# Kernel optimization log

Measured on AMD Instinct MI355X. Metric: run time of the kernel, lower is better.

## Reference

```python
import jax, jax.numpy as jnp
import numpy as np

NEG_SLOPE = 0.01  # torch nn.LeakyReLU default


def setup_inputs() -> dict:
    key = jax.random.key(0)
    k1, k2, k3 = jax.random.split(key, 3)
    B, H, D, L = 4, 8, 64, 2048
    q = jax.random.normal(k1, (B, H, D, L), dtype=jnp.float32)
    k = jax.random.normal(k2, (B, H, D, L), dtype=jnp.float32)
    v = jax.random.normal(k3, (B, H, D, L), dtype=jnp.float32)
    return {"q": q, "k": k, "v": v}


def reference(q, k, v):
    # q, k, v: [B, H, D, L] (note: feature dim BEFORE length, as in the torch module)
    d_tensor = q.shape[2]
    scale = 1.0 / np.sqrt(d_tensor).astype(np.float32)
    # scores = LeakyReLU(q^T k / sqrt(d)) : [B, H, Lq, Lk]
    scores = jnp.einsum('bhdq,bhdk->bhqk', q, k) * scale
    scores = jax.nn.leaky_relu(scores, negative_slope=NEG_SLOPE)
    psi = jax.nn.softmax(scores, axis=-1)
    # out = (psi @ v^T)^T : [B, H, D, Lq]
    out = jnp.einsum('bhqk,bhdk->bhdq', psi, v)
    return out
```

## Files before the change

kernel.cpp:

```cpp
#include <hip/hip_runtime.h>
#include <math.h>

#define DD 64
#define LL 2048
#define HEADS 32
#define TQ 128
#define TK 64
#define NTHREADS 512
#define QSCALE 0.18033688011112042f

typedef __bf16 bf16_t;
typedef __bf16 bf16x8 __attribute__((ext_vector_type(8)));
typedef float f32x16 __attribute__((ext_vector_type(16)));

__global__ __launch_bounds__(256)
void prep_bf16_kv(const float* __restrict__ k, const float* __restrict__ v,
                  bf16_t* __restrict__ kt, bf16_t* __restrict__ vb) {
  __shared__ float ld[64][65];
  const int t = threadIdx.x;
  const int which = blockIdx.z;
  const int head = blockIdx.y;
  const int l0 = blockIdx.x * 64;
  const size_t hoff = (size_t)head * DD * LL;
  if (which == 1) {
    const float* src = v + hoff;
    bf16_t* dst = vb + hoff;
    const int lp = (t & 31) * 2;
    const int db = (t >> 5) * 8;
    for (int i = 0; i < 8; ++i) {
      int d = db + i;
      float2 x = *(const float2*)(src + (size_t)d * LL + l0 + lp);
      union { bf16_t b[2]; unsigned u; } pk;
      pk.b[0] = (bf16_t)x.x;
      pk.b[1] = (bf16_t)x.y;
      *(unsigned*)(dst + (size_t)d * LL + l0 + lp) = pk.u;
    }
  } else {
    const float* src = k + hoff;
    bf16_t* dst = kt + hoff;
    const int l = t & 63;
    const int db = (t >> 6) * 16;
    for (int i = 0; i < 16; ++i) {
      int d = db + i;
      ld[l][d] = src[(size_t)d * LL + l0 + l];
    }
    __syncthreads();
    const int dp = (t & 31) * 2;
    const int lb = (t >> 5) * 8;
    for (int i = 0; i < 8; ++i) {
      int lw = lb + i;
      union { bf16_t b[2]; unsigned u; } pk;
      pk.b[0] = (bf16_t)ld[lw][dp];
      pk.b[1] = (bf16_t)ld[lw][dp + 1];
      *(unsigned*)(dst + (size_t)(l0 + lw) * DD + dp) = pk.u;
    }
  }
}

struct __align__(16) SMemA4 {
  union {
    bf16_t Qs[TQ][72];
    bf16_t Ks[2][TK][72];
  } qk;
  bf16_t Vs[2][DD][72];
};
union __align__(16) SMemU4 {
  SMemA4 a;
  float Oe[TQ][65];
};

__global__ __launch_bounds__(NTHREADS, 4)
void attn_flash_bf16_v5(const float* __restrict__ q, const bf16_t* __restrict__ kt,
                        const bf16_t* __restrict__ vb, float* __restrict__ out) {
  __shared__ SMemU4 sm;
  __shared__ float rs1[TQ];
  const int tid  = threadIdx.x;
  const int w    = tid >> 6;
  const int lane = tid & 63;
  const int l31  = lane & 31;
  const int hh   = lane >> 5;
  const int strip = w & 3;
  const int half  = w >> 2;
  const int wbase = strip * 32;
  const int lkh   = half * 32;
  const int bid  = blockIdx.x;
  const int j    = bid >> 3;
  const int head = (bid & 7) + 8 * (j >> 4);
  const int q0   = (j & 15) * TQ;
  const size_t hoff = (size_t)head * DD * LL;
  const float*  qp = q  + hoff;
  const bf16_t* kp = kt + hoff;
  const bf16_t* vp = vb + hoff;

  const int srow = tid >> 3;
  const int scol = (tid & 7) * 8;

  bf16x8 kreg = *(const bf16x8*)(kp + (size_t)srow * DD + scol);
  bf16x8 vreg = *(const bf16x8*)(vp + (size_t)srow * LL + scol);

  {
    int lq  = tid & 127;
    int d0q = (tid >> 7) * 16;
    const float* src = qp + q0 + lq;
    for (int g = 0; g < 2; ++g) {
      bf16x8 pk;
      for (int jj = 0; jj < 8; ++jj)
        pk[jj] = (bf16_t)(src[(size_t)(d0q + g * 8 + jj) * LL] * QSCALE);
      *(bf16x8*)&sm.a.qk.Qs[lq][d0q + g * 8] = pk;
    }
  }

  __syncthreads();
  bf16x8 bq[4];
  for (int kk = 0; kk < 4; ++kk)
    bq[kk] = *(const bf16x8*)&sm.a.qk.Qs[wbase + l31][kk * 16 + 8 * hh];
  __syncthreads();

  f32x16 oacc[2];
  for (int dt = 0; dt < 2; ++dt)
    for (int r = 0; r < 16; ++r) oacc[dt][r] = 0.f;
  float rsl[4];
  for (int i = 0; i < 4; ++i) rsl[i] = 0.f;

  for (int t = 0; t < LL / TK; ++t) {
    const int cur = t & 1;
    *(bf16x8*)&sm.a.qk.Ks[cur][srow][scol] = kreg;
    *(bf16x8*)&sm.a.Vs[cur][srow][scol]    = vreg;
    __syncthreads();

    if (t + 1 < LL / TK) {
      const int lk0n = (t + 1) * TK;
      kreg = *(const bf16x8*)(kp + (size_t)(lk0n + srow) * DD + scol);
      vreg = *(const bf16x8*)(vp + (size_t)srow * LL + lk0n + scol);
    }

    f32x16 st;
    for (int r = 0; r < 16; ++r) st[r] = 0.f;
    __builtin_amdgcn_s_setprio(1);
    for (int kk = 0; kk < 4; ++kk) {
      bf16x8 ak = *(const bf16x8*)&sm.a.qk.Ks[cur][lkh + l31][kk * 16 + 8 * hh];
      st = __builtin_amdgcn_mfma_f32_32x32x16_bf16(ak, bq[kk], st, 0, 0, 0);
    }
    __builtin_amdgcn_s_setprio(0);

    unsigned pb[8];
#pragma unroll
    for (int r = 0; r < 16; ++r) {
      float s = st[r];
      s = fmaxf(s, 0.01f * s);
      float p = __builtin_amdgcn_exp2f(s);
      rsl[r & 3] += p;
      st[r] = p;
    }
    for (int qq = 0; qq < 8; ++qq) {
      union { bf16_t b[2]; unsigned u; } pk;
      pk.b[0] = (bf16_t)st[2 * qq];
      pk.b[1] = (bf16_t)st[2 * qq + 1];
      pb[qq] = pk.u;
    }

    for (int kk2 = 0; kk2 < 2; ++kk2) {
      unsigned l0 = pb[4 * kk2 + 0], l1 = pb[4 * kk2 + 1];
      unsigned l2 = pb[4 * kk2 + 2], l3 = pb[4 * kk2 + 3];
      unsigned s0 = hh ? l0 : l2;
      unsigned s1 = hh ? l1 : l3;
      unsigned f0 = (unsigned)__shfl_xor((int)s0, 32);
      unsigned f1 = (unsigned)__shfl_xor((int)s1, 32);
      union { unsigned u[4]; bf16x8 v; } ap;
      ap.u[0] = hh ? f0 : l0;
      ap.u[1] = hh ? f1 : l1;
      ap.u[2] = hh ? l2 : f0;
      ap.u[3] = hh ? l3 : f1;
      const int lkb = lkh + kk2 * 16 + 8 * hh;
      __builtin_amdgcn_s_setprio(1);
      for (int dt = 0; dt < 2; ++dt) {
        bf16x8 bv = *(const bf16x8*)&sm.a.Vs[cur][dt * 32 + l31][lkb];
        oacc[dt] = __builtin_amdgcn_mfma_f32_32x32x16_bf16(ap.v, bv, oacc[dt], 0, 0, 0);
      }
      __builtin_amdgcn_s_setprio(0);
    }
  }

  float rsum = (rsl[0] + rsl[1]) + (rsl[2] + rsl[3]);
  float rtot = rsum + __shfl_xor(rsum, 32);
  __syncthreads();
  if (half == 1) {
    rs1[wbase + l31] = rtot;
    for (int r = 0; r < 16; ++r) {
      int row = (r & 3) + 8 * (r >> 2) + 4 * hh;
      for (int dt = 0; dt < 2; ++dt)
        sm.Oe[wbase + row][dt * 32 + l31] = oacc[dt][r];
    }
  }
  __syncthreads();
  if (half == 0) {
    float tot = rtot + rs1[wbase + l31];
    rs1[wbase + l31] = 1.0f / tot;
    float inv[16];
    for (int r = 0; r < 16; ++r) {
      int row = (r & 3) + 8 * (r >> 2) + 4 * hh;
      inv[r] = rs1[wbase + row];
    }
    for (int r = 0; r < 16; ++r) {
      int row = (r & 3) + 8 * (r >> 2) + 4 * hh;
      for (int dt = 0; dt < 2; ++dt) {
        int col = dt * 32 + l31;
        sm.Oe[wbase + row][col] = (oacc[dt][r] + sm.Oe[wbase + row][col]) * inv[r];
      }
    }
  }
  __syncthreads();
  float* op = out + hoff + q0;
  for (int i = 0; i < 16; ++i) {
    int idx = tid + NTHREADS * i;
    int d   = idx >> 7;
    int lq  = idx & 127;
    op[(size_t)d * LL + lq] = sm.Oe[lq][d];
  }
}

struct __align__(16) SMemA {
  bf16_t Qs[TQ][72];
  bf16_t Ks[TK][72];
  bf16_t Vs[DD][72];
};
union __align__(16) SMemU {
  SMemA a;
  float Oe[TQ][65];
};

__global__ __launch_bounds__(NTHREADS, 4)
void attn_flash_bf16(const float* __restrict__ q, const float* __restrict__ k,
                     const float* __restrict__ v, float* __restrict__ out) {
  __shared__ SMemU sm;
  __shared__ float rs1[TQ];
  const int tid  = threadIdx.x;
  const int w    = tid >> 6;
  const int lane = tid & 63;
  const int l31  = lane & 31;
  const int hh   = lane >> 5;
  const int strip = w & 3;
  const int half  = w >> 2;
  const int wbase = strip * 32;
  const int lkh   = half * 32;
  const int head = blockIdx.y;
  const int q0   = blockIdx.x * TQ;
  const size_t hoff = (size_t)head * DD * LL;
  const float* qp = q + hoff;
  const float* kp = k + hoff;
  const float* vp = v + hoff;

  {
    int lq  = tid & 127;
    int d0q = (tid >> 7) * 16;
    const float* src = qp + q0 + lq;
    for (int g = 0; g < 2; ++g) {
      bf16x8 pk;
      for (int jj = 0; jj < 8; ++jj)
        pk[jj] = (bf16_t)(src[(size_t)(d0q + g * 8 + jj) * LL] * QSCALE);
      *(bf16x8*)&sm.a.Qs[lq][d0q + g * 8] = pk;
    }
  }

  const int klk = tid & 63;
  const int kd0 = (tid >> 6) * 8;
  const int vd  = tid >> 3;
  const int vc8 = (tid & 7) * 8;

  float  kreg[8];
  float4 vreg[2];
  {
    const float* ks = kp + klk;
    for (int jj = 0; jj < 8; ++jj) kreg[jj] = ks[(size_t)(kd0 + jj) * LL];
    vreg[0] = *(const float4*)(vp + (size_t)vd * LL + vc8);
    vreg[1] = *(const float4*)(vp + (size_t)vd * LL + vc8 + 4);
  }

  __syncthreads();
  bf16x8 bq[4];
  for (int kk = 0; kk < 4; ++kk)
    bq[kk] = *(const bf16x8*)&sm.a.Qs[wbase + l31][kk * 16 + 8 * hh];

  f32x16 oacc[2];
  for (int dt = 0; dt < 2; ++dt)
    for (int r = 0; r < 16; ++r) oacc[dt][r] = 0.f;
  float rsum = 0.f;

  for (int t = 0; t < LL / TK; ++t) {
    __syncthreads();
    {
      bf16x8 pk;
      for (int jj = 0; jj < 8; ++jj) pk[jj] = (bf16_t)kreg[jj];
      *(bf16x8*)&sm.a.Ks[klk][kd0] = pk;
      bf16x8 pv;
      pv[0] = (bf16_t)vreg[0].x; pv[1] = (bf16_t)vreg[0].y;
      pv[2] = (bf16_t)vreg[0].z; pv[3] = (bf16_t)vreg[0].w;
      pv[4] = (bf16_t)vreg[1].x; pv[5] = (bf16_t)vreg[1].y;
      pv[6] = (bf16_t)vreg[1].z; pv[7] = (bf16_t)vreg[1].w;
      *(bf16x8*)&sm.a.Vs[vd][vc8] = pv;
    }
    __syncthreads();

    if (t + 1 < LL / TK) {
      const int lk0n = (t + 1) * TK;
      const float* ks = kp + lk0n + klk;
      for (int jj = 0; jj < 8; ++jj) kreg[jj] = ks[(size_t)(kd0 + jj) * LL];
      vreg[0] = *(const float4*)(vp + (size_t)vd * LL + lk0n + vc8);
      vreg[1] = *(const float4*)(vp + (size_t)vd * LL + lk0n + vc8 + 4);
    }

    f32x16 st;
    for (int r = 0; r < 16; ++r) st[r] = 0.f;
    for (int kk = 0; kk < 4; ++kk) {
      bf16x8 ak = *(const bf16x8*)&sm.a.Ks[lkh + l31][kk * 16 + 8 * hh];
      st = __builtin_amdgcn_mfma_f32_32x32x16_bf16(ak, bq[kk], st, 0, 0, 0);
    }

    unsigned pb[8];
    for (int r = 0; r < 16; ++r) {
      float s = st[r];
      s = fmaxf(s, 0.01f * s);
      float p = __builtin_amdgcn_exp2f(s);
      rsum += p;
      st[r] = p;
    }
    for (int qq = 0; qq < 8; ++qq) {
      union { bf16_t b[2]; unsigned u; } pk;
      pk.b[0] = (bf16_t)st[2 * qq];
      pk.b[1] = (bf16_t)st[2 * qq + 1];
      pb[qq] = pk.u;
    }

    for (int kk2 = 0; kk2 < 2; ++kk2) {
      unsigned l0 = pb[4 * kk2 + 0], l1 = pb[4 * kk2 + 1];
      unsigned l2 = pb[4 * kk2 + 2], l3 = pb[4 * kk2 + 3];
      unsigned s0 = hh ? l0 : l2;
      unsigned s1 = hh ? l1 : l3;
      unsigned f0 = (unsigned)__shfl_xor((int)s0, 32);
      unsigned f1 = (unsigned)__shfl_xor((int)s1, 32);
      union { unsigned u[4]; bf16x8 v; } ap;
      ap.u[0] = hh ? f0 : l0;
      ap.u[1] = hh ? f1 : l1;
      ap.u[2] = hh ? l2 : f0;
      ap.u[3] = hh ? l3 : f1;
      const int lkb = lkh + kk2 * 16 + 8 * hh;
      for (int dt = 0; dt < 2; ++dt) {
        bf16x8 bv = *(const bf16x8*)&sm.a.Vs[dt * 32 + l31][lkb];
        oacc[dt] = __builtin_amdgcn_mfma_f32_32x32x16_bf16(ap.v, bv, oacc[dt], 0, 0, 0);
      }
    }
  }

  float rtot = rsum + __shfl_xor(rsum, 32);
  __syncthreads();
  if (half == 1) {
    rs1[wbase + l31] = rtot;
    for (int r = 0; r < 16; ++r) {
      int row = (r & 3) + 8 * (r >> 2) + 4 * hh;
      for (int dt = 0; dt < 2; ++dt)
        sm.Oe[wbase + row][dt * 32 + l31] = oacc[dt][r];
    }
  }
  __syncthreads();
  if (half == 0) {
    float tot = rtot + rs1[wbase + l31];
    rs1[wbase + l31] = 1.0f / tot;
    float inv[16];
    for (int r = 0; r < 16; ++r) {
      int row = (r & 3) + 8 * (r >> 2) + 4 * hh;
      inv[r] = rs1[wbase + row];
    }
    for (int r = 0; r < 16; ++r) {
      int row = (r & 3) + 8 * (r >> 2) + 4 * hh;
      for (int dt = 0; dt < 2; ++dt) {
        int col = dt * 32 + l31;
        sm.Oe[wbase + row][col] = (oacc[dt][r] + sm.Oe[wbase + row][col]) * inv[r];
      }
    }
  }
  __syncthreads();
  float* op = out + hoff + q0;
  for (int i = 0; i < 16; ++i) {
    int idx = tid + NTHREADS * i;
    int d   = idx >> 7;
    int lq  = idx & 127;
    op[(size_t)d * LL + lq] = sm.Oe[lq][d];
  }
}

extern "C" void kernel_launch(void* const* d_in, const int* in_sizes, int n_in,
                              void* d_out, int out_size, void* d_ws, size_t ws_size,
                              hipStream_t stream) {
  const float* q = (const float*)d_in[0];
  const float* k = (const float*)d_in[1];
  const float* v = (const float*)d_in[2];
  float* out = (float*)d_out;
  const size_t per_buf = (size_t)HEADS * DD * LL;
  const size_t need = 2 * per_buf * sizeof(bf16_t);
  if (d_ws && ws_size >= need) {
    bf16_t* kt = (bf16_t*)d_ws;
    bf16_t* vb = kt + per_buf;
    prep_bf16_kv<<<dim3(LL / 64, HEADS, 2), 256, 0, stream>>>(k, v, kt, vb);
    attn_flash_bf16_v5<<<dim3((LL / TQ) * HEADS), NTHREADS, 0, stream>>>(q, kt, vb, out);
  } else {
    attn_flash_bf16<<<dim3(LL / TQ, HEADS), NTHREADS, 0, stream>>>(q, k, v, out);
  }
}
```

Before: 143.9 us.

## Split key dimension across two blocks and combine partial outputs in separate kernel

Adds a split-K variant of the flash attention kernel. Each query tile's key range is divided into two halves handled by separate blocks, which write unnormalized partial outputs and row sums to workspace. A new combine kernel adds the two partials, normalizes, and writes the transposed output. This doubles the block count (512 -> 1024) to improve occupancy across the CUs, at the cost of extra workspace traffic and an additional kernel launch. It relies on the no-max softmax (LeakyReLU scores are bounded), so the partials can be summed without rescaling.

```diff
diff --git a/kernel.cpp b/kernel.cpp
--- a/kernel.cpp
+++ b/kernel.cpp
@@ -7,6 +7,8 @@
 #define TQ 128
 #define TK 64
 #define NTHREADS 512
+#define NQT (LL / TQ)
+#define KHALF (LL / 2)
 #define QSCALE 0.18033688011112042f
 
 typedef __bf16 bf16_t;
@@ -68,6 +70,188 @@
   SMemA4 a;
   float Oe[TQ][65];
 };
+
+__global__ __launch_bounds__(NTHREADS, 4)
+void attn_flash_splitk(const float* __restrict__ q, const bf16_t* __restrict__ kt,
+                       const bf16_t* __restrict__ vb, float* __restrict__ po,
+                       float* __restrict__ pr) {
+  __shared__ SMemU4 sm;
+  __shared__ float rs1[TQ];
+  const int tid  = threadIdx.x;
+  const int w    = tid >> 6;
+  const int lane = tid & 63;
+  const int l31  = lane & 31;
+  const int hh   = lane >> 5;
+  const int strip = w & 3;
+  const int half  = w >> 2;
+  const int wbase = strip * 32;
+  const int lkh   = half * 32;
+  const int bid  = blockIdx.x;
+  const int j    = bid >> 3;
+  const int kp   = j & 1;
+  const int qt   = (j >> 1) & 15;
+  const int head = (bid & 7) + 8 * (j >> 5);
+  const int q0   = qt * TQ;
+  const int kbase = kp * KHALF;
+  const size_t hoff = (size_t)head * DD * LL;
+  const float*  qp = q  + hoff;
+  const bf16_t* kpt = kt + hoff;
+  const bf16_t* vp = vb + hoff;
+  const int b2 = ((head << 4) + qt) * 2 + kp;
+
+  const int srow = tid >> 3;
+  const int scol = (tid & 7) * 8;
+
+  bf16x8 kreg = *(const bf16x8*)(kpt + (size_t)(kbase + srow) * DD + scol);
+  bf16x8 vreg = *(const bf16x8*)(vp + (size_t)srow * LL + kbase + scol);
+
+  {
+    int lq  = tid & 127;
+    int d0q = (tid >> 7) * 16;
+    const float* src = qp + q0 + lq;
+    for (int g = 0; g < 2; ++g) {
+      bf16x8 pk;
+      for (int jj = 0; jj < 8; ++jj)
+        pk[jj] = (bf16_t)(src[(size_t)(d0q + g * 8 + jj) * LL] * QSCALE);
+      *(bf16x8*)&sm.a.qk.Qs[lq][d0q + g * 8] = pk;
+    }
+  }
+
+  __syncthreads();
+  bf16x8 bq[4];
+  for (int kk = 0; kk < 4; ++kk)
+    bq[kk] = *(const bf16x8*)&sm.a.qk.Qs[wbase + l31][kk * 16 + 8 * hh];
+  __syncthreads();
+
+  f32x16 oacc[2];
+  for (int dt = 0; dt < 2; ++dt)
+    for (int r = 0; r < 16; ++r) oacc[dt][r] = 0.f;
+  float rsl[4];
+  for (int i = 0; i < 4; ++i) rsl[i] = 0.f;
+
+  for (int t = 0; t < KHALF / TK; ++t) {
+    const int cur = t & 1;
+    *(bf16x8*)&sm.a.qk.Ks[cur][srow][scol] = kreg;
+    *(bf16x8*)&sm.a.Vs[cur][srow][scol]    = vreg;
+    __syncthreads();
+
+    if (t + 1 < KHALF / TK) {
+      const int lk0n = kbase + (t + 1) * TK;
+      kreg = *(const bf16x8*)(kpt + (size_t)(lk0n + srow) * DD + scol);
+      vreg = *(const bf16x8*)(vp + (size_t)srow * LL + lk0n + scol);
+    }
+
+    f32x16 st;
+    for (int r = 0; r < 16; ++r) st[r] = 0.f;
+    __builtin_amdgcn_s_setprio(1);
+    for (int kk = 0; kk < 4; ++kk) {
+      bf16x8 ak = *(const bf16x8*)&sm.a.qk.Ks[cur][lkh + l31][kk * 16 + 8 * hh];
+      st = __builtin_amdgcn_mfma_f32_32x32x16_bf16(ak, bq[kk], st, 0, 0, 0);
+    }
+    __builtin_amdgcn_s_setprio(0);
+
+    unsigned pb[8];
+#pragma unroll
+    for (int r = 0; r < 16; ++r) {
+      float s = st[r];
+      s = fmaxf(s, 0.01f * s);
+      float p = __builtin_amdgcn_exp2f(s);
+      rsl[r & 3] += p;
+      st[r] = p;
+    }
+    for (int qq = 0; qq < 8; ++qq) {
+      union { bf16_t b[2]; unsigned u; } pk;
+      pk.b[0] = (bf16_t)st[2 * qq];
+      pk.b[1] = (bf16_t)st[2 * qq + 1];
+      pb[qq] = pk.u;
+    }
+
+    for (int kk2 = 0; kk2 < 2; ++kk2) {
+      unsigned l0 = pb[4 * kk2 + 0], l1 = pb[4 * kk2 + 1];
+      unsigned l2 = pb[4 * kk2 + 2], l3 = pb[4 * kk2 + 3];
+      unsigned s0 = hh ? l0 : l2;
+      unsigned s1 = hh ? l1 : l3;
+      unsigned f0 = (unsigned)__shfl_xor((int)s0, 32);
+      unsigned f1 = (unsigned)__shfl_xor((int)s1, 32);
+      union { unsigned u[4]; bf16x8 v; } ap;
+      ap.u[0] = hh ? f0 : l0;
+      ap.u[1] = hh ? f1 : l1;
+      ap.u[2] = hh ? l2 : f0;
+      ap.u[3] = hh ? l3 : f1;
+      const int lkb = lkh + kk2 * 16 + 8 * hh;
+      __builtin_amdgcn_s_setprio(1);
+      for (int dt = 0; dt < 2; ++dt) {
+        bf16x8 bv = *(const bf16x8*)&sm.a.Vs[cur][dt * 32 + l31][lkb];
+        oacc[dt] = __builtin_amdgcn_mfma_f32_32x32x16_bf16(ap.v, bv, oacc[dt], 0, 0, 0);
+      }
+      __builtin_amdgcn_s_setprio(0);
+    }
+  }
+
+  float rsum = (rsl[0] + rsl[1]) + (rsl[2] + rsl[3]);
+  float rtot = rsum + __shfl_xor(rsum, 32);
+  __syncthreads();
+  if (half == 1) {
+    rs1[wbase + l31] = rtot;
+    for (int r = 0; r < 16; ++r) {
+      int row = (r & 3) + 8 * (r >> 2) + 4 * hh;
+      for (int dt = 0; dt < 2; ++dt)
+        sm.Oe[wbase + row][dt * 32 + l31] = oacc[dt][r];
+    }
+  }
+  __syncthreads();
+  if (half == 0) {
+    float tot = rtot + rs1[wbase + l31];
+    if (hh == 0) pr[(size_t)b2 * TQ + wbase + l31] = tot;
+    for (int r = 0; r < 16; ++r) {
+      int row = (r & 3) + 8 * (r >> 2) + 4 * hh;
+      for (int dt = 0; dt < 2; ++dt) {
+        int col = dt * 32 + l31;
+        sm.Oe[wbase + row][col] = oacc[dt][r] + sm.Oe[wbase + row][col];
+      }
+    }
+  }
+  __syncthreads();
+  float* pop = po + (size_t)b2 * (TQ * DD);
+  for (int i = 0; i < 16; ++i) {
+    int idx = tid + NTHREADS * i;
+    int lq = idx >> 6;
+    int d  = idx & 63;
+    pop[idx] = sm.Oe[lq][d];
+  }
+}
+
+__global__ __launch_bounds__(256)
+void combine_splitk(const float* __restrict__ po, const float* __restrict__ pr,
+                    float* __restrict__ out) {
+  __shared__ float Oe[TQ][65];
+  __shared__ float inv[TQ];
+  const int t = threadIdx.x;
+  const int b = blockIdx.x;
+  const int head = b >> 4;
+  const int q0   = (b & 15) * TQ;
+  const float* p0 = po + ((size_t)b * 2 + 0) * (TQ * DD);
+  const float* p1 = po + ((size_t)b * 2 + 1) * (TQ * DD);
+  for (int i = 0; i < (TQ * DD) / 256; ++i) {
+    int idx = t + 256 * i;
+    int lq = idx >> 6;
+    int d  = idx & 63;
+    Oe[lq][d] = p0[idx] + p1[idx];
+  }
+  if (t < TQ) {
+    const float* r0 = pr + ((size_t)b * 2 + 0) * TQ;
+    const float* r1 = pr + ((size_t)b * 2 + 1) * TQ;
+    inv[t] = 1.0f / (r0[t] + r1[t]);
+  }
+  __syncthreads();
+  float* op = out + (size_t)head * DD * LL + q0;
+  for (int i = 0; i < (TQ * DD) / 256; ++i) {
+    int idx = t + 256 * i;
+    int d  = idx >> 7;
+    int lq = idx & 127;
+    op[(size_t)d * LL + lq] = Oe[lq][d] * inv[lq];
+  }
+}
 
 __global__ __launch_bounds__(NTHREADS, 4)
 void attn_flash_bf16_v5(const float* __restrict__ q, const bf16_t* __restrict__ kt,
@@ -396,8 +580,19 @@
   const float* v = (const float*)d_in[2];
   float* out = (float*)d_out;
   const size_t per_buf = (size_t)HEADS * DD * LL;
-  const size_t need = 2 * per_buf * sizeof(bf16_t);
-  if (d_ws && ws_size >= need) {
+  const size_t kv_bytes = 2 * per_buf * sizeof(bf16_t);
+  const size_t po_elems = (size_t)HEADS * NQT * 2 * TQ * DD;
+  const size_t pr_elems = (size_t)HEADS * NQT * 2 * TQ;
+  const size_t need_full = kv_bytes + (po_elems + pr_elems) * sizeof(float);
+  if (d_ws && ws_size >= need_full) {
+    bf16_t* kt = (bf16_t*)d_ws;
+    bf16_t* vb = kt + per_buf;
+    float* po = (float*)((char*)d_ws + kv_bytes);
+    float* pr = po + po_elems;
+    prep_bf16_kv<<<dim3(LL / 64, HEADS, 2), 256, 0, stream>>>(k, v, kt, vb);
+    attn_flash_splitk<<<dim3(HEADS * NQT * 2), NTHREADS, 0, stream>>>(q, kt, vb, po, pr);
+    combine_splitk<<<dim3(HEADS * NQT), 256, 0, stream>>>(po, pr, out);
+  } else if (d_ws && ws_size >= kv_bytes) {
     bf16_t* kt = (bf16_t*)d_ws;
     bf16_t* vb = kt + per_buf;
     prep_bf16_kv<<<dim3(LL / 64, HEADS, 2), 256, 0, stream>>>(k, v, kt, vb);
```

Result: slower. 154.6 us (+7.4%).

## Load K/V MFMA fragments directly from global memory, dropping LDS staging

Applied to the files above, without the earlier changes.

The prep kernel now writes V in tiled 64x64 blocks, so each wave can fetch its MFMA operand fragments for K and V directly from global memory into registers. The attention loop no longer stages K/V tiles through shared memory and drops the per-iteration __syncthreads, prefetching the next tile's fragments into registers after the current MFMAs. Shared memory shrinks to the Q/output buffer, which may allow more resident blocks. The cost is that each of the 8 waves loads its own K/V fragments, adding redundant global/L2 traffic and more register pressure.

```diff
diff --git a/kernel.cpp b/kernel.cpp
--- a/kernel.cpp
+++ b/kernel.cpp
@@ -6,6 +6,7 @@
 #define HEADS 32
 #define TQ 128
 #define TK 64
+#define NT (LL / TK)
 #define NTHREADS 512
 #define QSCALE 0.18033688011112042f
 
@@ -14,8 +15,8 @@
 typedef float f32x16 __attribute__((ext_vector_type(16)));
 
 __global__ __launch_bounds__(256)
-void prep_bf16_kv(const float* __restrict__ k, const float* __restrict__ v,
-                  bf16_t* __restrict__ kt, bf16_t* __restrict__ vb) {
+void prep_bf16_kv2(const float* __restrict__ k, const float* __restrict__ v,
+                   bf16_t* __restrict__ kt, bf16_t* __restrict__ vt) {
   __shared__ float ld[64][65];
   const int t = threadIdx.x;
   const int which = blockIdx.z;
@@ -24,7 +25,7 @@
   const size_t hoff = (size_t)head * DD * LL;
   if (which == 1) {
     const float* src = v + hoff;
-    bf16_t* dst = vb + hoff;
+    bf16_t* dst = vt + hoff + (size_t)(l0 >> 6) * (DD * 64);
     const int lp = (t & 31) * 2;
     const int db = (t >> 5) * 8;
     for (int i = 0; i < 8; ++i) {
@@ -33,7 +34,7 @@
       union { bf16_t b[2]; unsigned u; } pk;
       pk.b[0] = (bf16_t)x.x;
       pk.b[1] = (bf16_t)x.y;
-      *(unsigned*)(dst + (size_t)d * LL + l0 + lp) = pk.u;
+      *(unsigned*)(dst + d * 64 + lp) = pk.u;
     }
   } else {
     const float* src = k + hoff;
@@ -57,22 +58,15 @@
   }
 }
 
-struct __align__(16) SMemA4 {
-  union {
-    bf16_t Qs[TQ][72];
-    bf16_t Ks[2][TK][72];
-  } qk;
-  bf16_t Vs[2][DD][72];
-};
-union __align__(16) SMemU4 {
-  SMemA4 a;
+union __align__(16) SMemU8 {
+  bf16_t Qs[TQ][72];
   float Oe[TQ][65];
 };
 
 __global__ __launch_bounds__(NTHREADS, 4)
-void attn_flash_bf16_v5(const float* __restrict__ q, const bf16_t* __restrict__ kt,
-                        const bf16_t* __restrict__ vb, float* __restrict__ out) {
-  __shared__ SMemU4 sm;
+void attn_flash_nolds(const float* __restrict__ q, const bf16_t* __restrict__ kt,
+                      const bf16_t* __restrict__ vt, float* __restrict__ out) {
+  __shared__ SMemU8 sm;
   __shared__ float rs1[TQ];
   const int tid  = threadIdx.x;
   const int w    = tid >> 6;
@@ -89,14 +83,17 @@
   const int q0   = (j & 15) * TQ;
   const size_t hoff = (size_t)head * DD * LL;
   const float*  qp = q  + hoff;
-  const bf16_t* kp = kt + hoff;
-  const bf16_t* vp = vb + hoff;
-
-  const int srow = tid >> 3;
-  const int scol = (tid & 7) * 8;
-
-  bf16x8 kreg = *(const bf16x8*)(kp + (size_t)srow * DD + scol);
-  bf16x8 vreg = *(const bf16x8*)(vp + (size_t)srow * LL + scol);
+
+  const bf16_t* kl = kt + hoff + (size_t)(lkh + l31) * 64 + hh * 8;
+  const bf16_t* vl = vt + hoff + (size_t)l31 * 64 + lkh + hh * 8;
+
+  bf16x8 ak[4], bv[4];
+#pragma unroll
+  for (int kk = 0; kk < 4; ++kk)
+    ak[kk] = *(const bf16x8*)(kl + kk * 16);
+#pragma unroll
+  for (int i = 0; i < 4; ++i)
+    bv[i] = *(const bf16x8*)(vl + (i >> 1) * 2048 + (i & 1) * 16);
 
   {
     int lq  = tid & 127;
@@ -106,15 +103,14 @@
       bf16x8 pk;
       for (int jj = 0; jj < 8; ++jj)
         pk[jj] = (bf16_t)(src[(size_t)(d0q + g * 8 + jj) * LL] * QSCALE);
-      *(bf16x8*)&sm.a.qk.Qs[lq][d0q + g * 8] = pk;
+      *(bf16x8*)&sm.Qs[lq][d0q + g * 8] = pk;
     }
   }
 
   __syncthreads();
   bf16x8 bq[4];
   for (int kk = 0; kk < 4; ++kk)
-    bq[kk] = *(const bf16x8*)&sm.a.qk.Qs[wbase + l31][kk * 16 + 8 * hh];
-  __syncthreads();
+    bq[kk] = *(const bf16x8*)&sm.Qs[wbase + l31][kk * 16 + 8 * hh];
 
   f32x16 oacc[2];
   for (int dt = 0; dt < 2; ++dt)
@@ -122,26 +118,19 @@
   float rsl[4];
   for (int i = 0; i < 4; ++i) rsl[i] = 0.f;
 
-  for (int t = 0; t < LL / TK; ++t) {
-    const int cur = t & 1;
-    *(bf16x8*)&sm.a.qk.Ks[cur][srow][scol] = kreg;
-    *(bf16x8*)&sm.a.Vs[cur][srow][scol]    = vreg;
-    __syncthreads();
-
-    if (t + 1 < LL / TK) {
-      const int lk0n = (t + 1) * TK;
-      kreg = *(const bf16x8*)(kp + (size_t)(lk0n + srow) * DD + scol);
-      vreg = *(const bf16x8*)(vp + (size_t)srow * LL + lk0n + scol);
-    }
+  for (int t = 0; t < NT; ++t) {
+    const int tn = (t + 1 < NT) ? t + 1 : t;
 
     f32x16 st;
     for (int r = 0; r < 16; ++r) st[r] = 0.f;
     __builtin_amdgcn_s_setprio(1);
-    for (int kk = 0; kk < 4; ++kk) {
-      bf16x8 ak = *(const bf16x8*)&sm.a.qk.Ks[cur][lkh + l31][kk * 16 + 8 * hh];
-      st = __builtin_amdgcn_mfma_f32_32x32x16_bf16(ak, bq[kk], st, 0, 0, 0);
-    }
+    for (int kk = 0; kk < 4; ++kk)
+      st = __builtin_amdgcn_mfma_f32_32x32x16_bf16(ak[kk], bq[kk], st, 0, 0, 0);
     __builtin_amdgcn_s_setprio(0);
+
+#pragma unroll
+    for (int kk = 0; kk < 4; ++kk)
+      ak[kk] = *(const bf16x8*)(kl + (size_t)tn * 4096 + kk * 16);
 
     unsigned pb[8];
 #pragma unroll
@@ -171,14 +160,16 @@
       ap.u[1] = hh ? f1 : l1;
       ap.u[2] = hh ? l2 : f0;
       ap.u[3] = hh ? l3 : f1;
-      const int lkb = lkh + kk2 * 16 + 8 * hh;
       __builtin_amdgcn_s_setprio(1);
-      for (int dt = 0; dt < 2; ++dt) {
-        bf16x8 bv = *(const bf16x8*)&sm.a.Vs[cur][dt * 32 + l31][lkb];
-        oacc[dt] = __builtin_amdgcn_mfma_f32_32x32x16_bf16(ap.v, bv, oacc[dt], 0, 0, 0);
-      }
+      for (int dt = 0; dt < 2; ++dt)
+        oacc[dt] = __builtin_amdgcn_mfma_f32_32x32x16_bf16(ap.v, bv[dt * 2 + kk2],
+                                                           oacc[dt], 0, 0, 0);
       __builtin_amdgcn_s_setprio(0);
     }
+
+#pragma unroll
+    for (int i = 0; i < 4; ++i)
+      bv[i] = *(const bf16x8*)(vl + (size_t)tn * 4096 + (i >> 1) * 2048 + (i & 1) * 16);
   }
 
   float rsum = (rsl[0] + rsl[1]) + (rsl[2] + rsl[3]);
@@ -312,8 +303,8 @@
     f32x16 st;
     for (int r = 0; r < 16; ++r) st[r] = 0.f;
     for (int kk = 0; kk < 4; ++kk) {
-      bf16x8 ak = *(const bf16x8*)&sm.a.Ks[lkh + l31][kk * 16 + 8 * hh];
-      st = __builtin_amdgcn_mfma_f32_32x32x16_bf16(ak, bq[kk], st, 0, 0, 0);
+      bf16x8 akf = *(const bf16x8*)&sm.a.Ks[lkh + l31][kk * 16 + 8 * hh];
+      st = __builtin_amdgcn_mfma_f32_32x32x16_bf16(akf, bq[kk], st, 0, 0, 0);
     }
 
     unsigned pb[8];
@@ -345,8 +336,8 @@
       ap.u[3] = hh ? l3 : f1;
       const int lkb = lkh + kk2 * 16 + 8 * hh;
       for (int dt = 0; dt < 2; ++dt) {
-        bf16x8 bv = *(const bf16x8*)&sm.a.Vs[dt * 32 + l31][lkb];
-        oacc[dt] = __builtin_amdgcn_mfma_f32_32x32x16_bf16(ap.v, bv, oacc[dt], 0, 0, 0);
+        bf16x8 bvf = *(const bf16x8*)&sm.a.Vs[dt * 32 + l31][lkb];
+        oacc[dt] = __builtin_amdgcn_mfma_f32_32x32x16_bf16(ap.v, bvf, oacc[dt], 0, 0, 0);
       }
     }
   }
@@ -399,9 +390,9 @@
   const size_t need = 2 * per_buf * sizeof(bf16_t);
   if (d_ws && ws_size >= need) {
     bf16_t* kt = (bf16_t*)d_ws;
-    bf16_t* vb = kt + per_buf;
-    prep_bf16_kv<<<dim3(LL / 64, HEADS, 2), 256, 0, stream>>>(k, v, kt, vb);
-    attn_flash_bf16_v5<<<dim3((LL / TQ) * HEADS), NTHREADS, 0, stream>>>(q, kt, vb, out);
+    bf16_t* vt = kt + per_buf;
+    prep_bf16_kv2<<<dim3(LL / 64, HEADS, 2), 256, 0, stream>>>(k, v, kt, vt);
+    attn_flash_nolds<<<dim3((LL / TQ) * HEADS), NTHREADS, 0, stream>>>(q, kt, vt, out);
   } else {
     attn_flash_bf16<<<dim3(LL / TQ, HEADS), NTHREADS, 0, stream>>>(q, k, v, out);
   }
```

Result: slower. 206.5 us (+43.5%).

## Software-pipeline QK^T one tile ahead of softmax and PV in flash kernel

Applied to the files above, without the earlier changes.

Restructures the main loop so that each iteration computes the QK^T scores for tile t while it applies softmax and the PV product to the scores of tile t-1. A prologue and an epilogue are added, and the V tile load lags K by one tile. The aim is to let the exp/pack VALU work and the PV MFMAs overlap with the next tile's score MFMAs and global loads. In exchange, a second 16-float score accumulator stays live, which raises register pressure and could hurt occupancy at 4 waves per SIMD.

```diff
diff --git a/kernel.cpp b/kernel.cpp
--- a/kernel.cpp
+++ b/kernel.cpp
@@ -6,6 +6,7 @@
 #define HEADS 32
 #define TQ 128
 #define TK 64
+#define NT (LL / TK)
 #define NTHREADS 512
 #define QSCALE 0.18033688011112042f
 
@@ -69,8 +70,51 @@
   float Oe[TQ][65];
 };
 
+#define SOFTMAX_PACK(STP, PB)                                  \
+  do {                                                         \
+    _Pragma("unroll")                                          \
+    for (int r = 0; r < 16; ++r) {                             \
+      float s = (STP)[r];                                      \
+      s = fmaxf(s, 0.01f * s);                                 \
+      float p = __builtin_amdgcn_exp2f(s);                     \
+      rsl[r & 3] += p;                                         \
+      (STP)[r] = p;                                            \
+    }                                                          \
+    for (int qq = 0; qq < 8; ++qq) {                           \
+      union { bf16_t b[2]; unsigned u; } pk;                   \
+      pk.b[0] = (bf16_t)(STP)[2 * qq];                         \
+      pk.b[1] = (bf16_t)(STP)[2 * qq + 1];                     \
+      (PB)[qq] = pk.u;                                         \
+    }                                                          \
+  } while (0)
+
+#define PV_STEP(PB, VS)                                                         \
+  do {                                                                          \
+    for (int kk2 = 0; kk2 < 2; ++kk2) {                                         \
+      unsigned l0 = (PB)[4 * kk2 + 0], l1 = (PB)[4 * kk2 + 1];                  \
+      unsigned l2 = (PB)[4 * kk2 + 2], l3 = (PB)[4 * kk2 + 3];                  \
+      unsigned s0 = hh ? l0 : l2;                                               \
+      unsigned s1 = hh ? l1 : l3;                                               \
+      unsigned f0 = (unsigned)__shfl_xor((int)s0, 32);                          \
+      unsigned f1 = (unsigned)__shfl_xor((int)s1, 32);                          \
+      union { unsigned u[4]; bf16x8 v; } ap;                                    \
+      ap.u[0] = hh ? f0 : l0;                                                   \
+      ap.u[1] = hh ? f1 : l1;                                                   \
+      ap.u[2] = hh ? l2 : f0;                                                   \
+      ap.u[3] = hh ? l3 : f1;                                                   \
+      const int lkb = lkh + kk2 * 16 + 8 * hh;                                  \
+      __builtin_amdgcn_s_setprio(1);                                            \
+      for (int dt = 0; dt < 2; ++dt) {                                          \
+        bf16x8 bv = *(const bf16x8*)&sm.a.Vs[VS][dt * 32 + l31][lkb];           \
+        oacc[dt] = __builtin_amdgcn_mfma_f32_32x32x16_bf16(ap.v, bv,            \
+                                                           oacc[dt], 0, 0, 0); \
+      }                                                                         \
+      __builtin_amdgcn_s_setprio(0);                                            \
+    }                                                                           \
+  } while (0)
+
 __global__ __launch_bounds__(NTHREADS, 4)
-void attn_flash_bf16_v5(const float* __restrict__ q, const bf16_t* __restrict__ kt,
+void attn_flash_bf16_v9(const float* __restrict__ q, const bf16_t* __restrict__ kt,
                         const bf16_t* __restrict__ vb, float* __restrict__ out) {
   __shared__ SMemU4 sm;
   __shared__ float rs1[TQ];
@@ -122,63 +166,54 @@
   float rsl[4];
   for (int i = 0; i < 4; ++i) rsl[i] = 0.f;
 
-  for (int t = 0; t < LL / TK; ++t) {
+  f32x16 stp;
+  {
+    *(bf16x8*)&sm.a.qk.Ks[0][srow][scol] = kreg;
+    __syncthreads();
+    for (int r = 0; r < 16; ++r) stp[r] = 0.f;
+    __builtin_amdgcn_s_setprio(1);
+    for (int kk = 0; kk < 4; ++kk) {
+      bf16x8 ak = *(const bf16x8*)&sm.a.qk.Ks[0][lkh + l31][kk * 16 + 8 * hh];
+      stp = __builtin_amdgcn_mfma_f32_32x32x16_bf16(ak, bq[kk], stp, 0, 0, 0);
+    }
+    __builtin_amdgcn_s_setprio(0);
+    kreg = *(const bf16x8*)(kp + (size_t)(TK + srow) * DD + scol);
+  }
+
+  for (int t = 1; t < NT; ++t) {
     const int cur = t & 1;
-    *(bf16x8*)&sm.a.qk.Ks[cur][srow][scol] = kreg;
-    *(bf16x8*)&sm.a.Vs[cur][srow][scol]    = vreg;
-    __syncthreads();
-
-    if (t + 1 < LL / TK) {
-      const int lk0n = (t + 1) * TK;
-      kreg = *(const bf16x8*)(kp + (size_t)(lk0n + srow) * DD + scol);
-      vreg = *(const bf16x8*)(vp + (size_t)srow * LL + lk0n + scol);
-    }
-
-    f32x16 st;
-    for (int r = 0; r < 16; ++r) st[r] = 0.f;
+    *(bf16x8*)&sm.a.qk.Ks[cur][srow][scol]  = kreg;
+    *(bf16x8*)&sm.a.Vs[cur ^ 1][srow][scol] = vreg;
+    __syncthreads();
+
+    f32x16 stc;
+    for (int r = 0; r < 16; ++r) stc[r] = 0.f;
     __builtin_amdgcn_s_setprio(1);
     for (int kk = 0; kk < 4; ++kk) {
       bf16x8 ak = *(const bf16x8*)&sm.a.qk.Ks[cur][lkh + l31][kk * 16 + 8 * hh];
-      st = __builtin_amdgcn_mfma_f32_32x32x16_bf16(ak, bq[kk], st, 0, 0, 0);
+      stc = __builtin_amdgcn_mfma_f32_32x32x16_bf16(ak, bq[kk], stc, 0, 0, 0);
     }
     __builtin_amdgcn_s_setprio(0);
 
+    {
+      const int tn = (t + 1 < NT) ? t + 1 : t;
+      kreg = *(const bf16x8*)(kp + (size_t)(tn * TK + srow) * DD + scol);
+      vreg = *(const bf16x8*)(vp + (size_t)srow * LL + t * TK + scol);
+    }
+
     unsigned pb[8];
-#pragma unroll
-    for (int r = 0; r < 16; ++r) {
-      float s = st[r];
-      s = fmaxf(s, 0.01f * s);
-      float p = __builtin_amdgcn_exp2f(s);
-      rsl[r & 3] += p;
-      st[r] = p;
-    }
-    for (int qq = 0; qq < 8; ++qq) {
-      union { bf16_t b[2]; unsigned u; } pk;
-      pk.b[0] = (bf16_t)st[2 * qq];
-      pk.b[1] = (bf16_t)st[2 * qq + 1];
-      pb[qq] = pk.u;
-    }
-
-    for (int kk2 = 0; kk2 < 2; ++kk2) {
-      unsigned l0 = pb[4 * kk2 + 0], l1 = pb[4 * kk2 + 1];
-      unsigned l2 = pb[4 * kk2 + 2], l3 = pb[4 * kk2 + 3];
-      unsigned s0 = hh ? l0 : l2;
-      unsigned s1 = hh ? l1 : l3;
-      unsigned f0 = (unsigned)__shfl_xor((int)s0, 32);
-      unsigned f1 = (unsigned)__shfl_xor((int)s1, 32);
-      union { unsigned u[4]; bf16x8 v; } ap;
-      ap.u[0] = hh ? f0 : l0;
-      ap.u[1] = hh ? f1 : l1;
-      ap.u[2] = hh ? l2 : f0;
-      ap.u[3] = hh ? l3 : f1;
-      const int lkb = lkh + kk2 * 16 + 8 * hh;
-      __builtin_amdgcn_s_setprio(1);
-      for (int dt = 0; dt < 2; ++dt) {
-        bf16x8 bv = *(const bf16x8*)&sm.a.Vs[cur][dt * 32 + l31][lkb];
-        oacc[dt] = __builtin_amdgcn_mfma_f32_32x32x16_bf16(ap.v, bv, oacc[dt], 0, 0, 0);
-      }
-      __builtin_amdgcn_s_setprio(0);
-    }
+    SOFTMAX_PACK(stp, pb);
+    PV_STEP(pb, cur ^ 1);
+
+    stp = stc;
+  }
+
+  {
+    *(bf16x8*)&sm.a.Vs[(NT - 1) & 1][srow][scol] = vreg;
+    __syncthreads();
+    unsigned pb[8];
+    SOFTMAX_PACK(stp, pb);
+    PV_STEP(pb, (NT - 1) & 1);
   }
 
   float rsum = (rsl[0] + rsl[1]) + (rsl[2] + rsl[3]);
@@ -312,8 +347,8 @@
     f32x16 st;
     for (int r = 0; r < 16; ++r) st[r] = 0.f;
     for (int kk = 0; kk < 4; ++kk) {
-      bf16x8 ak = *(const bf16x8*)&sm.a.Ks[lkh + l31][kk * 16 + 8 * hh];
-      st = __builtin_amdgcn_mfma_f32_32x32x16_bf16(ak, bq[kk], st, 0, 0, 0);
+      bf16x8 akf = *(const bf16x8*)&sm.a.Ks[lkh + l31][kk * 16 + 8 * hh];
+      st = __builtin_amdgcn_mfma_f32_32x32x16_bf16(akf, bq[kk], st, 0, 0, 0);
     }
 
     unsigned pb[8];
@@ -345,8 +380,8 @@
       ap.u[3] = hh ? l3 : f1;
       const int lkb = lkh + kk2 * 16 + 8 * hh;
       for (int dt = 0; dt < 2; ++dt) {
-        bf16x8 bv = *(const bf16x8*)&sm.a.Vs[dt * 32 + l31][lkb];
-        oacc[dt] = __builtin_amdgcn_mfma_f32_32x32x16_bf16(ap.v, bv, oacc[dt], 0, 0, 0);
+        bf16x8 bvf = *(const bf16x8*)&sm.a.Vs[dt * 32 + l31][lkb];
+        oacc[dt] = __builtin_amdgcn_mfma_f32_32x32x16_bf16(ap.v, bvf, oacc[dt], 0, 0, 0);
       }
     }
   }
@@ -401,7 +436,7 @@
     bf16_t* kt = (bf16_t*)d_ws;
     bf16_t* vb = kt + per_buf;
     prep_bf16_kv<<<dim3(LL / 64, HEADS, 2), 256, 0, stream>>>(k, v, kt, vb);
-    attn_flash_bf16_v5<<<dim3((LL / TQ) * HEADS), NTHREADS, 0, stream>>>(q, kt, vb, out);
+    attn_flash_bf16_v9<<<dim3((LL / TQ) * HEADS), NTHREADS, 0, stream>>>(q, kt, vb, out);
   } else {
     attn_flash_bf16<<<dim3(LL / TQ, HEADS), NTHREADS, 0, stream>>>(q, k, v, out);
   }
```

New measurement: 143.8 us. Within noise of the previous version (-0.1%).
